# Optimization experiments

Measured on AMD Instinct MI355X. Metric: run time of the kernel, lower is better.

Reference implementation:

```python
import jax, jax.numpy as jnp
import numpy as np

B, T, C = 8, 2048, 1024  # micro_bsz, seq_len, n_embd (== complexsize)


def setup_inputs() -> dict:
    key = jax.random.key(0)
    ks = jax.random.split(key, 6)
    w = lambda k, shape: (jax.random.normal(k, shape, dtype=jnp.float32) * 0.02)
    return {
        "x": jax.random.normal(ks[0], (B, T, C), dtype=jnp.float32),
        "Wk": w(ks[1], (2 * C, C)),      # key: n_embd -> 2*n_embd (no bias)
        "Wa": w(ks[2], (C, 2 * C)),      # activation: 2*n_embd -> n_embd (no bias)
        "Wf": w(ks[3], (2, C, C)),       # WaveNet filter conv, kernel=2, WIO layout
        "Wg": w(ks[4], (2, C, C)),       # WaveNet gate conv, kernel=2, WIO layout
        "Wo": w(ks[5], (C, C)),          # WaveNet 1x1 output projection
    }


def _causal_conv(x, W):
    # x: [B,T,Cin], W: [K,Cin,Cout]; left-pad K-1 for causality
    return jax.lax.conv_general_dilated(
        x, W, window_strides=(1,), padding=[(W.shape[0] - 1, 0)],
        dimension_numbers=("NWC", "WIO", "NWC"))


def _wavenet_short(x, Wf, Wg, Wo):
    # undialated gated WaveNet unit: tanh(conv_f(x)) * sigmoid(conv_g(x)) -> 1x1 proj
    h = jnp.tanh(_causal_conv(x, Wf)) * jax.nn.sigmoid(_causal_conv(x, Wg))
    return h @ Wo.T


def reference(x, Wk, Wa, Wf, Wg, Wo):
    Bx, Tx, Cx = x.shape
    k = (x @ Wk.T).reshape(Bx, Tx, Cx, 2)                 # [B,T,C,2]
    cv = jax.lax.complex(k[..., 0], k[..., 1])            # view_as_complex -> [B,T,C]
    scale = jax.lax.cummax(jnp.abs(cv), axis=1)           # running max of magnitude
    cv2 = cv / scale.astype(cv.dtype)                      # normalize magnitude <= 1
    kv = jnp.cumprod(cv2, axis=1)                          # complex cumulative product
    re = jnp.stack([kv.real, kv.imag], axis=-1).reshape(Bx, Tx, 2 * Cx)  # view_as_real
    return (re @ Wa.T) * _wavenet_short(x * scale, Wf, Wg, Wo)
```

## Files before the change

### kernel.cpp

```cpp
#include <hip/hip_runtime.h>
#include <cmath>

#define T_SEQ 2048
#define C_DIM 1024
#define BM 128
#define BN 128
#define BK 32

typedef unsigned short u16;
typedef unsigned int u32;
typedef short bf16x8 __attribute__((ext_vector_type(8)));
typedef _Float16 f16x8 __attribute__((ext_vector_type(8)));
typedef float f32x4 __attribute__((ext_vector_type(4)));
typedef unsigned short u16x8 __attribute__((ext_vector_type(8)));

#define AS1 __attribute__((address_space(1)))
#define AS3 __attribute__((address_space(3)))

__device__ __forceinline__ u16 f2bf(float f) {
    u32 u = __builtin_bit_cast(u32, f);
    u32 r = u + 0x7fffu + ((u >> 16) & 1u);
    return (u16)(r >> 16);
}
__device__ __forceinline__ u16 f2h(float f) {
    return __builtin_bit_cast(u16, (_Float16)f);
}
__device__ __forceinline__ float h2f(u16 h) {
    return (float)__builtin_bit_cast(_Float16, h);
}
__device__ __forceinline__ void gl_lds16(const void* g, void* l) {
    __builtin_amdgcn_global_load_lds((const AS1 u32*)g, (AS3 u32*)l, 16, 0, 0);
}

__device__ __forceinline__ int xcd_swz(int lin, int nwg) {
    return (lin & 7) * (nwg >> 3) + (lin >> 3);
}

#define SBAR() do { __builtin_amdgcn_sched_barrier(0); \
                    __builtin_amdgcn_s_barrier(); \
                    __builtin_amdgcn_sched_barrier(0); } while (0)
#define VMC(n) do { asm volatile("s_waitcnt vmcnt(" #n ")" ::: "memory"); \
                    __builtin_amdgcn_sched_barrier(0); } while (0)

__global__ __launch_bounds__(512, 2)
void gemm8(const u16* __restrict__ Ap, const u16* __restrict__ Bp,
           u16* __restrict__ Cout, int M, int N, int K)
{
    __shared__ u16 lds[2 * 32768];
    const int tid  = threadIdx.x;
    const int lane = tid & 63;
    const int wid  = tid >> 6;
    const int wrow = wid >> 2;
    const int wcol = wid & 3;
    const int gx = gridDim.x;
    const int lin = xcd_swz(blockIdx.x + gx * blockIdx.y, gx * gridDim.y);
    const int m0 = (lin / gx) * 256;
    const int n0 = (lin % gx) * 256;
    const int NT = K / 64;

    f32x4 acc[8][4] = {};

    auto stageu = [&](int t, int u) {
        const int isB = u & 1, kh = u >> 1;
        u16* ubase = &lds[(t & 1) * 32768 + isB * 16384 + kh * 8192];
        const u16* src = isB ? Bp + (size_t)n0 * K : Ap + (size_t)m0 * K;
        const int k0 = t * 64 + kh * 32;
        #pragma unroll
        for (int j = 0; j < 2; ++j) {
            const int c = wid + 8 * j;
            const int p = c * 64 + lane;
            const int row = p >> 2;
            const int sp  = (p & 3) ^ ((row >> 1) & 3);
            gl_lds16(src + (size_t)row * K + k0 + sp * 8, ubase + c * 512);
        }
    };

    auto lda = [&](int buf, int kh, int mq, f16x8 (&a)[4]) {
        const u16* base = &lds[buf * 32768 + kh * 8192];
        #pragma unroll
        for (int f = 0; f < 4; ++f) {
            const int row = wrow * 128 + mq * 64 + f * 16 + (lane & 15);
            const int sp  = (lane >> 4) ^ ((row >> 1) & 3);
            a[f] = *(const f16x8*)&base[row * 32 + sp * 8];
        }
    };
    auto ldb = [&](int buf, int kh, f16x8 (&b)[4]) {
        const u16* base = &lds[buf * 32768 + 16384 + kh * 8192];
        #pragma unroll
        for (int f = 0; f < 4; ++f) {
            const int row = wcol * 64 + f * 16 + (lane & 15);
            const int sp  = (lane >> 4) ^ ((row >> 1) & 3);
            b[f] = *(const f16x8*)&base[row * 32 + sp * 8];
        }
    };
    auto mm = [&](const f16x8 (&a)[4], const f16x8 (&b)[4], int mq) {
        __builtin_amdgcn_s_setprio(1);
        #pragma unroll
        for (int fm = 0; fm < 4; ++fm)
            #pragma unroll
            for (int fn = 0; fn < 4; ++fn)
                acc[mq * 4 + fm][fn] = __builtin_amdgcn_mfma_f32_16x16x32_f16(
                    a[fm], b[fn], acc[mq * 4 + fm][fn], 0, 0, 0);
        __builtin_amdgcn_s_setprio(0);
    };

    stageu(0, 0); stageu(0, 1); stageu(0, 2); stageu(0, 3);
    VMC(4);
    SBAR();

    f16x8 a[4], b[4];
    for (int t = 0; t < NT; ++t) {
        const int buf = t & 1;
        const bool more = (t + 1 < NT);
        if (more) { stageu(t + 1, 0); VMC(6); } else { VMC(4); }
        lda(buf, 0, 0, a); ldb(buf, 0, b);
        mm(a, b, 0);
        SBAR();
        if (more) stageu(t + 1, 1);
        lda(buf, 0, 1, a);
        mm(a, b, 1);
        SBAR();
        if (more) { stageu(t + 1, 2); VMC(6); } else { VMC(0); }
        lda(buf, 1, 0, a); ldb(buf, 1, b);
        mm(a, b, 0);
        SBAR();
        if (more) stageu(t + 1, 3);
        lda(buf, 1, 1, a);
        mm(a, b, 1);
        SBAR();
    }

    const int crow0 = m0 + wrow * 128 + ((lane >> 4) << 2);
    const int ccol  = n0 + wcol * 64 + (lane & 15);
    #pragma unroll
    for (int mi = 0; mi < 8; ++mi)
        #pragma unroll
        for (int fn = 0; fn < 4; ++fn)
            #pragma unroll
            for (int r = 0; r < 4; ++r)
                Cout[(size_t)(crow0 + mi * 16 + r) * N + ccol + fn * 16] =
                    f2h(acc[mi][fn][r]);
}

__global__ __launch_bounds__(512, 2)
void conv8(const u16* __restrict__ A, const u16* __restrict__ Wfgt,
           u16* __restrict__ H, int M)
{
    __shared__ u16 lds[2 * 32768];
    const int tid  = threadIdx.x;
    const int lane = tid & 63;
    const int wid  = tid >> 6;
    const int wrow = wid >> 2;
    const int wcol = wid & 3;
    const int gx = gridDim.x;
    const int lin = xcd_swz(blockIdx.x + gx * blockIdx.y, gx * gridDim.y);
    const int m0 = (lin / gx) * 256;
    const int n0 = (lin % gx) * 128;
    const int NT = 32;

    f32x4 accF[8][2] = {};
    f32x4 accG[8][2] = {};

    auto stageA = [&](int t, int kh) {
        u16* ubase = &lds[(t & 1) * 32768 + kh * 8192];
        const int tap = t >> 4;
        const int k0 = (t & 15) * 64 + kh * 32;
        const int sh = (tap == 0) ? 1 : 0;
        #pragma unroll
        for (int j = 0; j < 2; ++j) {
            const int c = wid + 8 * j;
            const int p = c * 64 + lane;
            const int row = p >> 2;
            const int sp  = (p & 3) ^ ((row >> 1) & 3);
            int grow = m0 + row - sh;
            if (grow < 0) grow = 0;
            gl_lds16(A + (size_t)grow * C_DIM + k0 + sp * 8, ubase + c * 512);
        }
    };
    auto stageB = [&](int t, int kh) {
        u16* ubase = &lds[(t & 1) * 32768 + 16384 + kh * 8192];
        const int tap = t >> 4;
        const int k0 = (t & 15) * 64 + kh * 32;
        const u16* BF = Wfgt + (size_t)tap * 2 * C_DIM * C_DIM;
        const u16* BG = BF + (size_t)C_DIM * C_DIM;
        #pragma unroll
        for (int j = 0; j < 2; ++j) {
            const int c = wid + 8 * j;
            const int isG = c >> 3;
            const int p = (c & 7) * 64 + lane;
            const int row = p >> 2;
            const int sp  = (p & 3) ^ ((row >> 1) & 3);
            const u16* src = (isG ? BG : BF) + (size_t)(n0 + row) * C_DIM + k0 + sp * 8;
            gl_lds16(src, ubase + isG * 4096 + (c & 7) * 512);
        }
    };

    auto lda8 = [&](int buf, int kh, bf16x8 (&a)[8]) {
        const u16* base = &lds[buf * 32768 + kh * 8192];
        #pragma unroll
        for (int f = 0; f < 8; ++f) {
            const int row = wrow * 128 + f * 16 + (lane & 15);
            const int sp  = (lane >> 4) ^ ((row >> 1) & 3);
            a[f] = *(const bf16x8*)&base[row * 32 + sp * 8];
        }
    };
    auto ldb2 = [&](int buf, int kh, int isG, bf16x8 (&b)[2]) {
        const u16* base = &lds[buf * 32768 + 16384 + kh * 8192 + isG * 4096];
        #pragma unroll
        for (int f = 0; f < 2; ++f) {
            const int row = wcol * 32 + f * 16 + (lane & 15);
            const int sp  = (lane >> 4) ^ ((row >> 1) & 3);
            b[f] = *(const bf16x8*)&base[row * 32 + sp * 8];
        }
    };
    auto mm2 = [&](const bf16x8 (&a)[8], const bf16x8 (&b)[2], f32x4 (&acc)[8][2]) {
        __builtin_amdgcn_s_setprio(1);
        #pragma unroll
        for (int fm = 0; fm < 8; ++fm)
            #pragma unroll
            for (int fn = 0; fn < 2; ++fn)
                acc[fm][fn] = __builtin_amdgcn_mfma_f32_16x16x32_bf16(
                    a[fm], b[fn], acc[fm][fn], 0, 0, 0);
        __builtin_amdgcn_s_setprio(0);
    };

    const bool zrow = (m0 % T_SEQ) == 0;

    auto zeroA = [&](int buf, int kh) {
        if (tid < 4) {
            u16x8 zz = {0,0,0,0,0,0,0,0};
            *(u16x8*)&lds[buf * 32768 + kh * 8192 + tid * 8] = zz;
        }
        asm volatile("s_waitcnt lgkmcnt(0)" ::: "memory");
        __builtin_amdgcn_sched_barrier(0);
        __builtin_amdgcn_s_barrier();
        __builtin_amdgcn_sched_barrier(0);
    };

    stageA(0, 0); stageB(0, 0); stageA(0, 1); stageB(0, 1);
    VMC(4);
    SBAR();

    bf16x8 a[8], bF[2], bG[2];
    for (int t = 0; t < NT; ++t) {
        const int buf = t & 1;
        const bool more = (t + 1 < NT);
        const bool z0 = zrow && (t < 16);
        if (more) { stageA(t + 1, 0); VMC(6); } else { VMC(4); }
        if (z0) zeroA(buf, 0);
        lda8(buf, 0, a); ldb2(buf, 0, 0, bF);
        mm2(a, bF, accF);
        SBAR();
        if (more) stageB(t + 1, 0);
        ldb2(buf, 0, 1, bG);
        mm2(a, bG, accG);
        SBAR();
        if (more) { stageA(t + 1, 1); VMC(6); } else { VMC(0); }
        if (z0) zeroA(buf, 1);
        lda8(buf, 1, a); ldb2(buf, 1, 0, bF);
        mm2(a, bF, accF);
        SBAR();
        if (more) stageB(t + 1, 1);
        ldb2(buf, 1, 1, bG);
        mm2(a, bG, accG);
        SBAR();
    }

    const int crow0 = m0 + wrow * 128 + ((lane >> 4) << 2);
    const int ccol  = n0 + wcol * 32 + (lane & 15);
    #pragma unroll
    for (int fm = 0; fm < 8; ++fm)
        #pragma unroll
        for (int fn = 0; fn < 2; ++fn)
            #pragma unroll
            for (int r = 0; r < 4; ++r) {
                const float fv = accF[fm][fn][r];
                const float gv = accG[fm][fn][r];
                const float th = 1.0f - 2.0f / (expf(2.0f * fv) + 1.0f);
                const float sg = 1.0f / (1.0f + expf(-gv));
                H[(size_t)(crow0 + fm * 16 + r) * C_DIM + ccol + fn * 16] = f2bf(th * sg);
            }
}

__global__ __launch_bounds__(256)
void dual_gemm(const u16* __restrict__ A1, const u16* __restrict__ B1, int K1,
               const u16* __restrict__ A2, const u16* __restrict__ B2, int K2,
               float* __restrict__ out, int M, int N)
{
    __shared__ u16 lds[2 * 2 * 4096];
    const int tid  = threadIdx.x;
    const int lane = tid & 63;
    const int wid  = tid >> 6;
    const int wr = wid >> 1, wc = wid & 1;
    const int gx = gridDim.x;
    const int lin = xcd_swz(blockIdx.x + gx * blockIdx.y, gx * gridDim.y);
    const int m0 = (lin / gx) * BM;
    const int n0 = (lin % gx) * BN;

    f32x4 acc1[4][4] = {};
    f32x4 acc2[4][4] = {};

    auto stage = [&](const u16* Ap, const u16* Bp, int K, int it, int buf) {
        const int k0 = it * BK;
        u16* base = &lds[buf * 8192];
        #pragma unroll
        for (int i = 0; i < 2; ++i) {
            const int chunk = wid + 4 * i;
            const int rloc  = chunk * 16 + (lane >> 2);
            const int slot  = (lane & 3) ^ ((rloc >> 1) & 3);
            gl_lds16(Bp + (size_t)(n0 + rloc) * K + k0 + slot * 8,
                     base + 4096 + chunk * 512);
            gl_lds16(Ap + (size_t)(m0 + rloc) * K + k0 + slot * 8,
                     base + chunk * 512);
        }
    };

    auto compute = [&](int buf, f32x4 (&acc)[4][4]) {
        const u16* base = &lds[buf * 8192];
        bf16x8 a[4], b[4];
        #pragma unroll
        for (int f = 0; f < 4; ++f) {
            const int row = wr * 64 + f * 16 + (lane & 15);
            const int sp  = ((lane >> 4) & 3) ^ ((row >> 1) & 3);
            a[f] = *(const bf16x8*)&base[row * 32 + sp * 8];
            const int rowb = wc * 64 + f * 16 + (lane & 15);
            const int spb  = ((lane >> 4) & 3) ^ ((rowb >> 1) & 3);
            b[f] = *(const bf16x8*)&base[4096 + rowb * 32 + spb * 8];
        }
        #pragma unroll
        for (int fm = 0; fm < 4; ++fm)
            #pragma unroll
            for (int fn = 0; fn < 4; ++fn)
                acc[fm][fn] = __builtin_amdgcn_mfma_f32_16x16x32_bf16(a[fm], b[fn], acc[fm][fn], 0, 0, 0);
    };

    const int NT1 = K1 / BK, NT2 = K2 / BK;
    stage(A1, B1, K1, 0, 0);
    int cur = 0;
    for (int it = 0; it < NT1; ++it) {
        __syncthreads();
        if (it + 1 < NT1) stage(A1, B1, K1, it + 1, cur ^ 1);
        else              stage(A2, B2, K2, 0, cur ^ 1);
        compute(cur, acc1);
        cur ^= 1;
    }
    for (int it = 0; it < NT2; ++it) {
        __syncthreads();
        if (it + 1 < NT2) stage(A2, B2, K2, it + 1, cur ^ 1);
        compute(cur, acc2);
        cur ^= 1;
    }

    const int crow0 = m0 + wr * 64 + ((lane >> 4) << 2);
    const int ccol  = n0 + wc * 64 + (lane & 15);
    #pragma unroll
    for (int fm = 0; fm < 4; ++fm)
        #pragma unroll
        for (int fn = 0; fn < 4; ++fn)
            #pragma unroll
            for (int r = 0; r < 4; ++r) {
                const size_t idx = (size_t)(crow0 + fm * 16 + r) * N + ccol + fn * 16;
                out[idx] = acc1[fm][fn][r] * acc2[fm][fn][r];
            }
}

#define SSEG 32
#define SCHB 32
#define SSL (T_SEQ / SSEG)

__global__ __launch_bounds__(1024, 1)
void scan_kernel(u16* __restrict__ kq, u16* __restrict__ xyb)
{
    __shared__ float  lmax[SSEG][SCHB];
    __shared__ float2 lprod[SSEG][SCHB];
    const int blk = blockIdx.x;
    const int b   = blk >> 5;
    const int c0  = (blk & 31) * SCHB;
    const int ch  = threadIdx.x & (SCHB - 1);
    const int seg = threadIdx.x >> 5;
    const int c   = c0 + ch;
    const int t0  = seg * SSL;
    const size_t baseh = (size_t)b * T_SEQ * 2048 + 2 * c + (size_t)t0 * 2048;
    const size_t base1 = (size_t)b * T_SEQ * C_DIM + c + (size_t)t0 * C_DIM;

    float m2 = 0.f;
    {
        size_t idx = baseh;
        for (int t = 0; t < SSL; ++t) {
            const u32 v = *(const u32*)&kq[idx];
            const float re = h2f((u16)(v & 0xffffu));
            const float im = h2f((u16)(v >> 16));
            m2 = fmaxf(m2, re * re + im * im);
            idx += 2048;
        }
    }
    lmax[seg][ch] = sqrtf(m2);
    __syncthreads();
    #pragma unroll
    for (int s = 1; s < SSEG; s <<= 1) {
        const float v = lmax[seg][ch];
        const float u = (seg >= s) ? lmax[seg - s][ch] : 0.f;
        __syncthreads();
        lmax[seg][ch] = fmaxf(v, u);
        __syncthreads();
    }
    const float premax = (seg > 0) ? lmax[seg - 1][ch] : 0.f;

    float pr = 1.f, pi = 0.f;
    float m = premax;
    {
        size_t idx = baseh, idx1 = base1;
        for (int t = 0; t < SSL; ++t) {
            const u32 v = *(const u32*)&kq[idx];
            const float re = h2f((u16)(v & 0xffffu));
            const float im = h2f((u16)(v >> 16));
            m = fmaxf(m, sqrtf(re * re + im * im));
            const float inv = 1.f / m;
            const float r0 = re * inv, r1 = im * inv;
            const float nr = pr * r0 - pi * r1;
            const float ni = pr * r1 + pi * r0;
            pr = nr; pi = ni;
            const float xv = h2f(xyb[idx1]);
            xyb[idx1] = f2bf(xv * m);
            idx += 2048; idx1 += C_DIM;
        }
    }
    lprod[seg][ch] = make_float2(pr, pi);
    __syncthreads();
    #pragma unroll
    for (int s = 1; s < SSEG; s <<= 1) {
        const float2 v = lprod[seg][ch];
        const float2 u = (seg >= s) ? lprod[seg - s][ch] : make_float2(1.f, 0.f);
        __syncthreads();
        lprod[seg][ch] = make_float2(u.x * v.x - u.y * v.y,
                                     u.x * v.y + u.y * v.x);
        __syncthreads();
    }
    float ppr = 1.f, ppi = 0.f;
    if (seg > 0) { const float2 pp = lprod[seg - 1][ch]; ppr = pp.x; ppi = pp.y; }

    pr = 1.f; pi = 0.f;
    m = premax;
    {
        size_t idx = baseh;
        for (int t = 0; t < SSL; ++t) {
            const u32 v = *(const u32*)&kq[idx];
            const float re = h2f((u16)(v & 0xffffu));
            const float im = h2f((u16)(v >> 16));
            m = fmaxf(m, sqrtf(re * re + im * im));
            const float inv = 1.f / m;
            const float r0 = re * inv, r1 = im * inv;
            const float nr = pr * r0 - pi * r1;
            const float ni = pr * r1 + pi * r0;
            pr = nr; pi = ni;
            const float fr = ppr * nr - ppi * ni;
            const float fi = ppr * ni + ppi * nr;
            *(u32*)&kq[idx] = ((u32)f2bf(fi) << 16) | (u32)f2bf(fr);
            idx += 2048;
        }
    }
}

__global__ void cvt_weights(const float* __restrict__ Wk, const float* __restrict__ Wa,
                            const float* __restrict__ Wo, u16* __restrict__ Wkh,
                            u16* __restrict__ Wab, u16* __restrict__ Wob)
{
    const int n1 = 2048 * 1024, n2 = 2 * 2048 * 1024, n3 = n2 + 1024 * 1024;
    const int i = (blockIdx.x * blockDim.x + threadIdx.x) * 4;
    if (i < n1) {
        const float4 v = *(const float4*)&Wk[i];
        ushort4 o; o.x = f2h(v.x); o.y = f2h(v.y); o.z = f2h(v.z); o.w = f2h(v.w);
        *(ushort4*)&Wkh[i] = o;
    } else if (i < n2) {
        const int j = i - n1;
        const float4 v = *(const float4*)&Wa[j];
        ushort4 o; o.x = f2bf(v.x); o.y = f2bf(v.y); o.z = f2bf(v.z); o.w = f2bf(v.w);
        *(ushort4*)&Wab[j] = o;
    } else if (i < n3) {
        const int j = i - n2;
        const float4 v = *(const float4*)&Wo[j];
        ushort4 o; o.x = f2bf(v.x); o.y = f2bf(v.y); o.z = f2bf(v.z); o.w = f2bf(v.w);
        *(ushort4*)&Wob[j] = o;
    }
}

__global__ void cvt_f16(const float* __restrict__ src, u16* __restrict__ dst, int n)
{
    const int i = (blockIdx.x * blockDim.x + threadIdx.x) * 4;
    if (i >= n) return;
    const float4 v = *(const float4*)&src[i];
    ushort4 o;
    o.x = f2h(v.x); o.y = f2h(v.y); o.z = f2h(v.z); o.w = f2h(v.w);
    *(ushort4*)&dst[i] = o;
}

__global__ __launch_bounds__(256)
void wtrans(const float* __restrict__ Wf, const float* __restrict__ Wg,
            u16* __restrict__ dst)
{
    __shared__ float tile[64][65];
    const int z = blockIdx.z;
    const float* src = ((z < 2) ? Wf : Wg) + (size_t)(z & 1) * C_DIM * C_DIM;
    u16* d = dst + (size_t)(z & 1) * (2 * C_DIM) * C_DIM
                 + ((z < 2) ? (size_t)0 : (size_t)C_DIM * C_DIM);
    const int k0 = blockIdx.x * 64;
    const int n0 = blockIdx.y * 64;
    const int tx = threadIdx.x & 63, ty = threadIdx.x >> 6;
    #pragma unroll
    for (int i = 0; i < 16; ++i) {
        const int r = ty + i * 4;
        tile[r][tx] = src[(size_t)(k0 + r) * C_DIM + n0 + tx];
    }
    __syncthreads();
    #pragma unroll
    for (int i = 0; i < 16; ++i) {
        const int r = ty + i * 4;
        d[(size_t)(n0 + r) * C_DIM + k0 + tx] = f2bf(tile[tx][r]);
    }
}

extern "C" void kernel_launch(void* const* d_in, const int* in_sizes, int n_in,
                              void* d_out, int out_size, void* d_ws, size_t ws_size,
                              hipStream_t stream)
{
    const float* x  = (const float*)d_in[0];
    const float* Wk = (const float*)d_in[1];
    const float* Wa = (const float*)d_in[2];
    const float* Wf = (const float*)d_in[3];
    const float* Wg = (const float*)d_in[4];
    const float* Wo = (const float*)d_in[5];
    float* out = (float*)d_out;

    const int M = 8 * T_SEQ;
    u16* kq   = (u16*)d_ws;
    u16* yb   = (u16*)((char*)d_ws + 67108864ull);
    u16* hb   = (u16*)((char*)d_ws + 100663296ull);
    u16* Wkh  = (u16*)((char*)d_ws + 134217728ull);
    u16* Wab  = Wkh + 2048 * 1024;
    u16* Wfgt = Wab + 2048 * 1024;
    u16* Wob  = Wfgt + 2ull * 2048 * 1024;

    cvt_weights<<<(5 * 1024 * 1024 / 4 + 255) / 256, 256, 0, stream>>>(
        Wk, Wa, Wo, Wkh, Wab, Wob);
    wtrans  <<<dim3(16, 16, 4), 256, 0, stream>>>(Wf, Wg, Wfgt);
    cvt_f16 <<<(M * 1024 / 4) / 256, 256, 0, stream>>>(x, yb, M * 1024);

    gemm8<<<dim3(2048 / 256, M / 256), 512, 0, stream>>>(
        yb, Wkh, kq, M, 2048, 1024);

    scan_kernel<<<256, 1024, 0, stream>>>(kq, yb);

    conv8<<<dim3(1024 / 128, M / 256), 512, 0, stream>>>(yb, Wfgt, hb, M);

    dual_gemm<<<dim3(1024 / BN, M / BM), 256, 0, stream>>>(
        kq, Wab, 2048, hb, Wob, 1024, out, M, 1024);
}
```

Baseline: 450.3 us.

## Reorder GEMM/conv pipeline: issue LDS reads before prefetch, zero causal row in registers

Restructures the main loops of the gemm8 and conv8 kernels so LDS fragment reads are issued before the next tile's global-to-LDS prefetch. Each phase now adds an extra barrier plus an lgkmcnt(0) wait, and the vmcnt waits move to the second and fourth phases. In conv8 the causal-padding zero row is no longer written into LDS behind its own barrier; the affected lane zeroes its A fragment in registers instead. The aim is to overlap global loads with LDS reads and drop the zeroing barriers, at the cost of more barriers per iteration.

```diff
diff --git a/kernel.cpp b/kernel.cpp
--- a/kernel.cpp
+++ b/kernel.cpp
@@ -41,6 +41,8 @@
                     __builtin_amdgcn_sched_barrier(0); } while (0)
 #define VMC(n) do { asm volatile("s_waitcnt vmcnt(" #n ")" ::: "memory"); \
                     __builtin_amdgcn_sched_barrier(0); } while (0)
+#define LGKM0() do { asm volatile("s_waitcnt lgkmcnt(0)" ::: "memory"); \
+                     __builtin_amdgcn_sched_barrier(0); } while (0)
 
 __global__ __launch_bounds__(512, 2)
 void gemm8(const u16* __restrict__ Ap, const u16* __restrict__ Bp,
@@ -105,27 +107,31 @@
     };
 
     stageu(0, 0); stageu(0, 1); stageu(0, 2); stageu(0, 3);
-    VMC(4);
+    VMC(0);
     SBAR();
 
     f16x8 a[4], b[4];
     for (int t = 0; t < NT; ++t) {
         const int buf = t & 1;
         const bool more = (t + 1 < NT);
-        if (more) { stageu(t + 1, 0); VMC(6); } else { VMC(4); }
         lda(buf, 0, 0, a); ldb(buf, 0, b);
+        if (more) stageu(t + 1, 0);
+        SBAR(); LGKM0();
         mm(a, b, 0);
         SBAR();
-        if (more) stageu(t + 1, 1);
         lda(buf, 0, 1, a);
+        if (more) { stageu(t + 1, 1); VMC(4); } else { VMC(0); }
+        SBAR(); LGKM0();
         mm(a, b, 1);
         SBAR();
-        if (more) { stageu(t + 1, 2); VMC(6); } else { VMC(0); }
         lda(buf, 1, 0, a); ldb(buf, 1, b);
+        if (more) stageu(t + 1, 2);
+        SBAR(); LGKM0();
         mm(a, b, 0);
         SBAR();
-        if (more) stageu(t + 1, 3);
         lda(buf, 1, 1, a);
+        if (more) { stageu(t + 1, 3); VMC(4); }
+        SBAR(); LGKM0();
         mm(a, b, 1);
         SBAR();
     }
@@ -225,20 +231,11 @@
     };
 
     const bool zrow = (m0 % T_SEQ) == 0;
-
-    auto zeroA = [&](int buf, int kh) {
-        if (tid < 4) {
-            u16x8 zz = {0,0,0,0,0,0,0,0};
-            *(u16x8*)&lds[buf * 32768 + kh * 8192 + tid * 8] = zz;
-        }
-        asm volatile("s_waitcnt lgkmcnt(0)" ::: "memory");
-        __builtin_amdgcn_sched_barrier(0);
-        __builtin_amdgcn_s_barrier();
-        __builtin_amdgcn_sched_barrier(0);
-    };
+    const bool zlane = (wrow == 0) && ((lane & 15) == 0);
+    const bf16x8 zvec = {0,0,0,0,0,0,0,0};
 
     stageA(0, 0); stageB(0, 0); stageA(0, 1); stageB(0, 1);
-    VMC(4);
+    VMC(0);
     SBAR();
 
     bf16x8 a[8], bF[2], bG[2];
@@ -246,22 +243,26 @@
         const int buf = t & 1;
         const bool more = (t + 1 < NT);
         const bool z0 = zrow && (t < 16);
-        if (more) { stageA(t + 1, 0); VMC(6); } else { VMC(4); }
-        if (z0) zeroA(buf, 0);
         lda8(buf, 0, a); ldb2(buf, 0, 0, bF);
+        if (more) stageA(t + 1, 0);
+        SBAR(); LGKM0();
+        if (z0 && zlane) a[0] = zvec;
         mm2(a, bF, accF);
         SBAR();
-        if (more) stageB(t + 1, 0);
         ldb2(buf, 0, 1, bG);
+        if (more) { stageB(t + 1, 0); VMC(4); } else { VMC(0); }
+        SBAR(); LGKM0();
         mm2(a, bG, accG);
         SBAR();
-        if (more) { stageA(t + 1, 1); VMC(6); } else { VMC(0); }
-        if (z0) zeroA(buf, 1);
         lda8(buf, 1, a); ldb2(buf, 1, 0, bF);
+        if (more) stageA(t + 1, 1);
+        SBAR(); LGKM0();
+        if (z0 && zlane) a[0] = zvec;
         mm2(a, bF, accF);
         SBAR();
-        if (more) stageB(t + 1, 1);
         ldb2(buf, 1, 1, bG);
+        if (more) { stageB(t + 1, 1); VMC(4); }
+        SBAR(); LGKM0();
         mm2(a, bG, accG);
         SBAR();
     }
```

After: 450.9 us. No clear change (+0.1%).
